# Optimization experiments

Hardware: AMD Instinct MI355X
Metric: run time of the kernel (lower is better)

Reference implementation:

```python
import jax, jax.numpy as jnp
import numpy as np
import math

B, C, H, W, S = 8, 512, 64, 64, 4


def setup_inputs() -> dict:
    key = jax.random.key(0)
    ks = jax.random.split(key, 7)
    s = 1.0 / math.sqrt(C)  # ~ torch Linear init scale
    x = jax.random.normal(ks[0], (B, C, H, W), jnp.float32)
    Wq = jax.random.uniform(ks[1], (C, C), jnp.float32, -s, s)
    bq = jax.random.uniform(ks[2], (C,), jnp.float32, -s, s)
    Wk = jax.random.uniform(ks[3], (C, C), jnp.float32, -s, s)
    bk = jax.random.uniform(ks[4], (C,), jnp.float32, -s, s)
    Wv = jax.random.uniform(ks[5], (C, C), jnp.float32, -s, s)
    bv = jax.random.uniform(ks[6], (C,), jnp.float32, -s, s)
    return {"x": x, "Wq": Wq, "bq": bq, "Wk": Wk, "bk": bk, "Wv": Wv, "bv": bv}


def reference(x, Wq, bq, Wk, bk, Wv, bv):
    # x: (B, C, H, W). Faithful to the torch module's output, but expressed
    # in the algebraically-equivalent efficient form: the repeat_interleaved
    # attention matrix A is block-constant, so out = repeat(A_m @ Vsum).
    b, c, h, w = x.shape
    nb = (h // S) * (w // S)  # number of SxS spatial blocks
    hw = h * w
    ss = S * S

    # Block means in unfold order (bh, bw): (B, nb, C)
    x_avg = x.reshape(b, c, h // S, S, w // S, S).mean(axis=(3, 5))
    x_avg = x_avg.reshape(b, c, nb).transpose(0, 2, 1)

    Q = x_avg @ Wq.T + bq  # (B, nb, C)
    K = x_avg @ Wk.T + bk  # (B, nb, C)
    A = jax.nn.softmax(jnp.einsum('bnc,bmc->bnm', Q, K) / jnp.sqrt(jnp.float32(c)), axis=-1)

    # V over flat row-major pixels: (B, HW, C)
    x_flat = x.reshape(b, c, hw).transpose(0, 2, 1)
    V = x_flat @ Wv.T + bv

    # repeat_interleave on dim=2 means column group j of A sums V rows
    # [j*ss, (j+1)*ss) in FLAT pixel order (not spatial blocks) - faithful.
    Vsum = V.reshape(b, hw // ss, ss, c).sum(axis=2)  # (B, nb, C)
    out_small = jnp.einsum('bnm,bmc->bnc', A, Vsum)   # (B, nb, C)
    # repeat_interleave on dim=1: each block row broadcast to ss flat pixels
    out_flat = jnp.repeat(out_small, ss, axis=1)      # (B, HW, C)
    return out_flat.transpose(0, 2, 1).reshape(b, c, h, w)
```

## Files before the change

kernel.cpp:

```cpp
#include <hip/hip_runtime.h>

typedef __attribute__((ext_vector_type(8))) short short8;
typedef __attribute__((ext_vector_type(4))) float f32x4;

__device__ __forceinline__ unsigned short f2bf(float f) {
    union { float f; unsigned int i; } v; v.f = f;
    unsigned int x = v.i;
    return (unsigned short)((x + 0x7FFFu + ((x >> 16) & 1u)) >> 16);
}
__device__ __forceinline__ f32x4 mfma16(short8 a, short8 b, f32x4 c) {
    return __builtin_amdgcn_mfma_f32_16x16x32_bf16(a, b, c, 0, 0, 0);
}

__global__ void prep_kernel(const float* __restrict__ x,
                            const float* __restrict__ Wq,
                            const float* __restrict__ Wk,
                            const float* __restrict__ Wv,
                            unsigned short* __restrict__ xavg,
                            unsigned short* __restrict__ xsum,
                            unsigned short* __restrict__ Wb)
{
    const int blk = blockIdx.x;
    const int t = threadIdx.x;
    if (blk >= 4096) {
        const int i = (blk - 4096) * 256 + t;
        const int m = i >> 15;
        const int o = (i & 32767) * 8;
        const float* src = (m == 0) ? Wq : (m == 1) ? Wk : Wv;
        unsigned short* dst = Wb + m * 262144 + o;
        float4 a = *(const float4*)(src + o);
        float4 b = *(const float4*)(src + o + 4);
        *(ushort4*)(dst)     = make_ushort4(f2bf(a.x), f2bf(a.y), f2bf(a.z), f2bf(a.w));
        *(ushort4*)(dst + 4) = make_ushort4(f2bf(b.x), f2bf(b.y), f2bf(b.z), f2bf(b.w));
        return;
    }
    const int b = blk >> 9;
    const int c = blk & 511;

    const float4* p = (const float4*)(x + (size_t)blk * 4096) + t * 4;
    float4 a0 = p[0], a1 = p[1], a2 = p[2], a3 = p[3];
    float s0 = a0.x + a0.y + a0.z + a0.w;
    float s1 = a1.x + a1.y + a1.z + a1.w;
    float s2 = a2.x + a2.y + a2.z + a2.w;
    float s3 = a3.x + a3.y + a3.z + a3.w;

    xsum[((size_t)b * 256 + t) * 512 + c] = f2bf(s0 + s1 + s2 + s3);

    __shared__ float part[1024];
    ((float4*)part)[t] = make_float4(s0, s1, s2, s3);
    __syncthreads();

    const int bh = t >> 4, bw = t & 15;
    float m = (part[(bh * 4 + 0) * 16 + bw] + part[(bh * 4 + 1) * 16 + bw] +
               part[(bh * 4 + 2) * 16 + bw] + part[(bh * 4 + 3) * 16 + bw]) * 0.0625f;
    xavg[((size_t)b * 256 + t) * 512 + c] = f2bf(m);
}

__global__ void qk_gemm(const unsigned short* __restrict__ X,
                        const unsigned short* __restrict__ Wqk,
                        const float* __restrict__ bq,
                        const float* __restrict__ bk,
                        unsigned short* __restrict__ QK)
{
    const int wave = blockIdx.x * 4 + (threadIdx.x >> 6);
    const int mt2 = wave >> 5, nt2 = wave & 31;
    const int lane = threadIdx.x & 63, quad = lane >> 4, r16 = lane & 15;
    const unsigned short* xp0 = X + (size_t)(mt2 * 32 + r16) * 512 + quad * 8;
    const unsigned short* xp1 = xp0 + 16 * 512;
    const unsigned short* wp0 = Wqk + (size_t)(nt2 * 32 + r16) * 512 + quad * 8;
    const unsigned short* wp1 = wp0 + 16 * 512;

    f32x4 acc00 = {0,0,0,0}, acc01 = acc00, acc10 = acc00, acc11 = acc00;
#pragma unroll 4
    for (int k = 0; k < 512; k += 32) {
        short8 a0 = *(const short8*)(xp0 + k);
        short8 a1 = *(const short8*)(xp1 + k);
        short8 b0 = *(const short8*)(wp0 + k);
        short8 b1 = *(const short8*)(wp1 + k);
        acc00 = mfma16(a0, b0, acc00);
        acc01 = mfma16(a0, b1, acc01);
        acc10 = mfma16(a1, b0, acc10);
        acc11 = mfma16(a1, b1, acc11);
    }
    const int c0 = nt2 * 32 + r16, c1 = c0 + 16;
    const float bias0 = (c0 < 512) ? bq[c0] : bk[c0 - 512];
    const float bias1 = (c1 < 512) ? bq[c1] : bk[c1 - 512];
    const int row0 = mt2 * 32 + quad * 4;
#pragma unroll
    for (int r = 0; r < 4; ++r) {
        QK[(size_t)(row0 + r) * 1024 + c0]      = f2bf(acc00[r] + bias0);
        QK[(size_t)(row0 + r) * 1024 + c1]      = f2bf(acc01[r] + bias1);
        QK[(size_t)(row0 + 16 + r) * 1024 + c0] = f2bf(acc10[r] + bias0);
        QK[(size_t)(row0 + 16 + r) * 1024 + c1] = f2bf(acc11[r] + bias1);
    }
}

__global__ void v_gemm(const unsigned short* __restrict__ xsum,
                       const unsigned short* __restrict__ Wvb,
                       const float* __restrict__ bv,
                       unsigned short* __restrict__ VsT)
{
    const int b = blockIdx.y;
    const int wave = blockIdx.x * 4 + (threadIdx.x >> 6);
    const int mt2 = wave >> 4, nt2 = wave & 15;
    const int lane = threadIdx.x & 63, quad = lane >> 4, r16 = lane & 15;
    const unsigned short* xp0 = xsum + (size_t)b * 131072 + (size_t)(mt2 * 32 + r16) * 512 + quad * 8;
    const unsigned short* xp1 = xp0 + 16 * 512;
    const unsigned short* wp0 = Wvb + (size_t)(nt2 * 32 + r16) * 512 + quad * 8;
    const unsigned short* wp1 = wp0 + 16 * 512;

    f32x4 acc00 = {0,0,0,0}, acc01 = acc00, acc10 = acc00, acc11 = acc00;
#pragma unroll 4
    for (int k = 0; k < 512; k += 32) {
        short8 a0 = *(const short8*)(xp0 + k);
        short8 a1 = *(const short8*)(xp1 + k);
        short8 b0 = *(const short8*)(wp0 + k);
        short8 b1 = *(const short8*)(wp1 + k);
        acc00 = mfma16(a0, b0, acc00);
        acc01 = mfma16(a0, b1, acc01);
        acc10 = mfma16(a1, b0, acc10);
        acc11 = mfma16(a1, b1, acc11);
    }
    const int c0 = nt2 * 32 + r16, c1 = c0 + 16;
    const float bias0 = 16.f * bv[c0], bias1 = 16.f * bv[c1];
    unsigned short* vb = VsT + (size_t)b * 131072;
    const int m0 = mt2 * 32 + quad * 4;
#pragma unroll
    for (int r = 0; r < 4; ++r) {
        vb[(size_t)c0 * 256 + m0 + r]      = f2bf(acc00[r] + bias0);
        vb[(size_t)c1 * 256 + m0 + r]      = f2bf(acc01[r] + bias1);
        vb[(size_t)c0 * 256 + m0 + 16 + r] = f2bf(acc10[r] + bias0);
        vb[(size_t)c1 * 256 + m0 + 16 + r] = f2bf(acc11[r] + bias1);
    }
}

__global__ void score_softmax(const unsigned short* __restrict__ QK,
                              unsigned short* __restrict__ Amat)
{
    __shared__ float S[32][257];
    const int b = blockIdx.y, strip = blockIdx.x;
    const int w = threadIdx.x >> 6, lane = threadIdx.x & 63;
    const int quad = lane >> 4, r16 = lane & 15;
    const unsigned short* qp0 = QK + (size_t)(b * 256 + strip * 32 + r16) * 1024 + quad * 8;
    const unsigned short* qp1 = qp0 + 16 * 1024;

#pragma unroll
    for (int g = 0; g < 2; ++g) {
        const int ct = w * 2 + g;
        const unsigned short* kp0 = QK + (size_t)(b * 256 + ct * 32 + r16) * 1024 + 512 + quad * 8;
        const unsigned short* kp1 = kp0 + 16 * 1024;
        f32x4 acc00 = {0,0,0,0}, acc01 = acc00, acc10 = acc00, acc11 = acc00;
#pragma unroll 4
        for (int k = 0; k < 512; k += 32) {
            short8 a0 = *(const short8*)(qp0 + k);
            short8 a1 = *(const short8*)(qp1 + k);
            short8 b0 = *(const short8*)(kp0 + k);
            short8 b1 = *(const short8*)(kp1 + k);
            acc00 = mfma16(a0, b0, acc00);
            acc01 = mfma16(a0, b1, acc01);
            acc10 = mfma16(a1, b0, acc10);
            acc11 = mfma16(a1, b1, acc11);
        }
        const int col0 = ct * 32 + r16;
#pragma unroll
        for (int r = 0; r < 4; ++r) {
            S[quad * 4 + r][col0]           = acc00[r];
            S[quad * 4 + r][col0 + 16]      = acc01[r];
            S[quad * 4 + 16 + r][col0]      = acc10[r];
            S[quad * 4 + 16 + r][col0 + 16] = acc11[r];
        }
    }
    __syncthreads();

    const int t = threadIdx.x;
    const int r = t >> 3, seg = t & 7;
    float v[32];
    float mx = -3.4e38f;
#pragma unroll
    for (int j = 0; j < 32; ++j) {
        v[j] = S[r][seg * 32 + j] * 0.044194173824159216f;
        mx = fmaxf(mx, v[j]);
    }
    mx = fmaxf(mx, __shfl_xor(mx, 1));
    mx = fmaxf(mx, __shfl_xor(mx, 2));
    mx = fmaxf(mx, __shfl_xor(mx, 4));
    float sum = 0.f;
#pragma unroll
    for (int j = 0; j < 32; ++j) { v[j] = __expf(v[j] - mx); sum += v[j]; }
    sum += __shfl_xor(sum, 1);
    sum += __shfl_xor(sum, 2);
    sum += __shfl_xor(sum, 4);
    const float inv = 1.f / sum;
    unsigned short* ap = Amat + (size_t)b * 65536 + (size_t)(strip * 32 + r) * 256 + seg * 32;
#pragma unroll
    for (int j = 0; j < 32; j += 4)
        *(ushort4*)(ap + j) = make_ushort4(f2bf(v[j] * inv), f2bf(v[j + 1] * inv),
                                           f2bf(v[j + 2] * inv), f2bf(v[j + 3] * inv));
}

__global__ void av_expand(const unsigned short* __restrict__ Amat,
                          const unsigned short* __restrict__ VsT,
                          float* __restrict__ out)
{
    const int b = blockIdx.y;
    const int wave = blockIdx.x * 4 + (threadIdx.x >> 6);
    const int mt2 = wave >> 4, nt2 = wave & 15;
    const int lane = threadIdx.x & 63, quad = lane >> 4, r16 = lane & 15;
    const unsigned short* ap0 = Amat + (size_t)b * 65536 + (size_t)(mt2 * 32 + r16) * 256 + quad * 8;
    const unsigned short* ap1 = ap0 + 16 * 256;
    const unsigned short* vp0 = VsT + (size_t)b * 131072 + (size_t)(nt2 * 32 + r16) * 256 + quad * 8;
    const unsigned short* vp1 = vp0 + 16 * 256;

    f32x4 acc00 = {0,0,0,0}, acc01 = acc00, acc10 = acc00, acc11 = acc00;
#pragma unroll 4
    for (int k = 0; k < 256; k += 32) {
        short8 a0 = *(const short8*)(ap0 + k);
        short8 a1 = *(const short8*)(ap1 + k);
        short8 b0 = *(const short8*)(vp0 + k);
        short8 b1 = *(const short8*)(vp1 + k);
        acc00 = mfma16(a0, b0, acc00);
        acc01 = mfma16(a0, b1, acc01);
        acc10 = mfma16(a1, b0, acc10);
        acc11 = mfma16(a1, b1, acc11);
    }
    const int c0 = nt2 * 32 + r16, c1 = c0 + 16;
    float* ob0 = out + (size_t)(b * 512 + c0) * 4096;
    float* ob1 = out + (size_t)(b * 512 + c1) * 4096;
    const int n0 = mt2 * 32 + quad * 4;
#pragma unroll
    for (int r = 0; r < 4; ++r) {
        float4 q;
        float4* d;
        q = make_float4(acc00[r], acc00[r], acc00[r], acc00[r]);
        d = (float4*)(ob0 + (n0 + r) * 16);      d[0] = q; d[1] = q; d[2] = q; d[3] = q;
        q = make_float4(acc01[r], acc01[r], acc01[r], acc01[r]);
        d = (float4*)(ob1 + (n0 + r) * 16);      d[0] = q; d[1] = q; d[2] = q; d[3] = q;
        q = make_float4(acc10[r], acc10[r], acc10[r], acc10[r]);
        d = (float4*)(ob0 + (n0 + 16 + r) * 16); d[0] = q; d[1] = q; d[2] = q; d[3] = q;
        q = make_float4(acc11[r], acc11[r], acc11[r], acc11[r]);
        d = (float4*)(ob1 + (n0 + 16 + r) * 16); d[0] = q; d[1] = q; d[2] = q; d[3] = q;
    }
}

extern "C" void kernel_launch(void* const* d_in, const int* in_sizes, int n_in,
                              void* d_out, int out_size, void* d_ws, size_t ws_size,
                              hipStream_t stream) {
    const float* x  = (const float*)d_in[0];
    const float* Wq = (const float*)d_in[1];
    const float* bq = (const float*)d_in[2];
    const float* Wk = (const float*)d_in[3];
    const float* bk = (const float*)d_in[4];
    const float* Wv = (const float*)d_in[5];
    const float* bv = (const float*)d_in[6];
    float* out = (float*)d_out;

    unsigned short* so   = (unsigned short*)d_out;
    unsigned short* Wb   = so;
    unsigned short* xavg = Wb + 786432;
    unsigned short* xsum = xavg + 1048576;
    unsigned short* QK   = xsum + 1048576;
    unsigned short* VsT  = (unsigned short*)d_ws;
    unsigned short* Amat = VsT + 1048576;

    prep_kernel<<<4480, 256, 0, stream>>>(x, Wq, Wk, Wv, xavg, xsum, Wb);
    qk_gemm<<<512, 256, 0, stream>>>(xavg, Wb, bq, bk, QK);
    v_gemm<<<dim3(32, 8), 256, 0, stream>>>(xsum, Wb + 524288, bv, VsT);
    score_softmax<<<dim3(8, 8), 256, 0, stream>>>(QK, Amat);
    av_expand<<<dim3(32, 8), 256, 0, stream>>>(Amat, VsT, out);
}
```

Before: 199.7 us.

## Merge projection GEMMs into one launch and fuse softmax with AV expand

The QK and V projection GEMMs now run as one kernel, with the block index choosing the branch, so they share a single launch. Score computation, softmax and the A·V expand are fused into one kernel, and the attention matrix stays in shared memory instead of going through global memory. To do this, each score strip is recomputed by four blocks, one per quarter of the channels, which repeats the QK^T work four times. All intermediates now live in the workspace rather than partly in the output buffer.

```diff
diff --git a/kernel.cpp b/kernel.cpp
--- a/kernel.cpp
+++ b/kernel.cpp
@@ -56,94 +56,100 @@
     xavg[((size_t)b * 256 + t) * 512 + c] = f2bf(m);
 }
 
-__global__ void qk_gemm(const unsigned short* __restrict__ X,
-                        const unsigned short* __restrict__ Wqk,
-                        const float* __restrict__ bq,
-                        const float* __restrict__ bk,
-                        unsigned short* __restrict__ QK)
+__global__ void proj_gemm(const unsigned short* __restrict__ xavg,
+                          const unsigned short* __restrict__ xsum,
+                          const unsigned short* __restrict__ Wb,
+                          const float* __restrict__ bq,
+                          const float* __restrict__ bk,
+                          const float* __restrict__ bv,
+                          unsigned short* __restrict__ QK,
+                          unsigned short* __restrict__ VsT)
 {
-    const int wave = blockIdx.x * 4 + (threadIdx.x >> 6);
-    const int mt2 = wave >> 5, nt2 = wave & 31;
+    const int blk = blockIdx.x;
     const int lane = threadIdx.x & 63, quad = lane >> 4, r16 = lane & 15;
-    const unsigned short* xp0 = X + (size_t)(mt2 * 32 + r16) * 512 + quad * 8;
-    const unsigned short* xp1 = xp0 + 16 * 512;
-    const unsigned short* wp0 = Wqk + (size_t)(nt2 * 32 + r16) * 512 + quad * 8;
-    const unsigned short* wp1 = wp0 + 16 * 512;
-
-    f32x4 acc00 = {0,0,0,0}, acc01 = acc00, acc10 = acc00, acc11 = acc00;
-#pragma unroll 4
-    for (int k = 0; k < 512; k += 32) {
-        short8 a0 = *(const short8*)(xp0 + k);
-        short8 a1 = *(const short8*)(xp1 + k);
-        short8 b0 = *(const short8*)(wp0 + k);
-        short8 b1 = *(const short8*)(wp1 + k);
-        acc00 = mfma16(a0, b0, acc00);
-        acc01 = mfma16(a0, b1, acc01);
-        acc10 = mfma16(a1, b0, acc10);
-        acc11 = mfma16(a1, b1, acc11);
-    }
-    const int c0 = nt2 * 32 + r16, c1 = c0 + 16;
-    const float bias0 = (c0 < 512) ? bq[c0] : bk[c0 - 512];
-    const float bias1 = (c1 < 512) ? bq[c1] : bk[c1 - 512];
-    const int row0 = mt2 * 32 + quad * 4;
-#pragma unroll
-    for (int r = 0; r < 4; ++r) {
-        QK[(size_t)(row0 + r) * 1024 + c0]      = f2bf(acc00[r] + bias0);
-        QK[(size_t)(row0 + r) * 1024 + c1]      = f2bf(acc01[r] + bias1);
-        QK[(size_t)(row0 + 16 + r) * 1024 + c0] = f2bf(acc10[r] + bias0);
-        QK[(size_t)(row0 + 16 + r) * 1024 + c1] = f2bf(acc11[r] + bias1);
-    }
-}
-
-__global__ void v_gemm(const unsigned short* __restrict__ xsum,
-                       const unsigned short* __restrict__ Wvb,
-                       const float* __restrict__ bv,
-                       unsigned short* __restrict__ VsT)
-{
-    const int b = blockIdx.y;
-    const int wave = blockIdx.x * 4 + (threadIdx.x >> 6);
-    const int mt2 = wave >> 4, nt2 = wave & 15;
-    const int lane = threadIdx.x & 63, quad = lane >> 4, r16 = lane & 15;
-    const unsigned short* xp0 = xsum + (size_t)b * 131072 + (size_t)(mt2 * 32 + r16) * 512 + quad * 8;
-    const unsigned short* xp1 = xp0 + 16 * 512;
-    const unsigned short* wp0 = Wvb + (size_t)(nt2 * 32 + r16) * 512 + quad * 8;
-    const unsigned short* wp1 = wp0 + 16 * 512;
-
-    f32x4 acc00 = {0,0,0,0}, acc01 = acc00, acc10 = acc00, acc11 = acc00;
-#pragma unroll 4
-    for (int k = 0; k < 512; k += 32) {
-        short8 a0 = *(const short8*)(xp0 + k);
-        short8 a1 = *(const short8*)(xp1 + k);
-        short8 b0 = *(const short8*)(wp0 + k);
-        short8 b1 = *(const short8*)(wp1 + k);
-        acc00 = mfma16(a0, b0, acc00);
-        acc01 = mfma16(a0, b1, acc01);
-        acc10 = mfma16(a1, b0, acc10);
-        acc11 = mfma16(a1, b1, acc11);
-    }
-    const int c0 = nt2 * 32 + r16, c1 = c0 + 16;
-    const float bias0 = 16.f * bv[c0], bias1 = 16.f * bv[c1];
-    unsigned short* vb = VsT + (size_t)b * 131072;
-    const int m0 = mt2 * 32 + quad * 4;
-#pragma unroll
-    for (int r = 0; r < 4; ++r) {
-        vb[(size_t)c0 * 256 + m0 + r]      = f2bf(acc00[r] + bias0);
-        vb[(size_t)c1 * 256 + m0 + r]      = f2bf(acc01[r] + bias1);
-        vb[(size_t)c0 * 256 + m0 + 16 + r] = f2bf(acc10[r] + bias0);
-        vb[(size_t)c1 * 256 + m0 + 16 + r] = f2bf(acc11[r] + bias1);
-    }
-}
-
-__global__ void score_softmax(const unsigned short* __restrict__ QK,
-                              unsigned short* __restrict__ Amat)
+    const int w = threadIdx.x >> 6;
+
+    if (blk < 512) {
+        const int wave = blk * 4 + w;
+        const int mt2 = wave >> 5, nt2 = wave & 31;
+        const unsigned short* xp0 = xavg + (size_t)(mt2 * 32 + r16) * 512 + quad * 8;
+        const unsigned short* xp1 = xp0 + 16 * 512;
+        const unsigned short* wp0 = Wb + (size_t)(nt2 * 32 + r16) * 512 + quad * 8;
+        const unsigned short* wp1 = wp0 + 16 * 512;
+
+        f32x4 acc00 = {0,0,0,0}, acc01 = acc00, acc10 = acc00, acc11 = acc00;
+#pragma unroll 4
+        for (int k = 0; k < 512; k += 32) {
+            short8 a0 = *(const short8*)(xp0 + k);
+            short8 a1 = *(const short8*)(xp1 + k);
+            short8 b0 = *(const short8*)(wp0 + k);
+            short8 b1 = *(const short8*)(wp1 + k);
+            acc00 = mfma16(a0, b0, acc00);
+            acc01 = mfma16(a0, b1, acc01);
+            acc10 = mfma16(a1, b0, acc10);
+            acc11 = mfma16(a1, b1, acc11);
+        }
+        const int c0 = nt2 * 32 + r16, c1 = c0 + 16;
+        const float bias0 = (c0 < 512) ? bq[c0] : bk[c0 - 512];
+        const float bias1 = (c1 < 512) ? bq[c1] : bk[c1 - 512];
+        const int row0 = mt2 * 32 + quad * 4;
+#pragma unroll
+        for (int r = 0; r < 4; ++r) {
+            QK[(size_t)(row0 + r) * 1024 + c0]      = f2bf(acc00[r] + bias0);
+            QK[(size_t)(row0 + r) * 1024 + c1]      = f2bf(acc01[r] + bias1);
+            QK[(size_t)(row0 + 16 + r) * 1024 + c0] = f2bf(acc10[r] + bias0);
+            QK[(size_t)(row0 + 16 + r) * 1024 + c1] = f2bf(acc11[r] + bias1);
+        }
+    } else {
+        const int vblk = blk - 512;
+        const int b = vblk >> 5;
+        const int wave = (vblk & 31) * 4 + w;
+        const int mt2 = wave >> 4, nt2 = wave & 15;
+        const unsigned short* xp0 = xsum + (size_t)b * 131072 + (size_t)(mt2 * 32 + r16) * 512 + quad * 8;
+        const unsigned short* xp1 = xp0 + 16 * 512;
+        const unsigned short* wp0 = Wb + 524288 + (size_t)(nt2 * 32 + r16) * 512 + quad * 8;
+        const unsigned short* wp1 = wp0 + 16 * 512;
+
+        f32x4 acc00 = {0,0,0,0}, acc01 = acc00, acc10 = acc00, acc11 = acc00;
+#pragma unroll 4
+        for (int k = 0; k < 512; k += 32) {
+            short8 a0 = *(const short8*)(xp0 + k);
+            short8 a1 = *(const short8*)(xp1 + k);
+            short8 b0 = *(const short8*)(wp0 + k);
+            short8 b1 = *(const short8*)(wp1 + k);
+            acc00 = mfma16(a0, b0, acc00);
+            acc01 = mfma16(a0, b1, acc01);
+            acc10 = mfma16(a1, b0, acc10);
+            acc11 = mfma16(a1, b1, acc11);
+        }
+        const int c0 = nt2 * 32 + r16, c1 = c0 + 16;
+        const float bias0 = 16.f * bv[c0], bias1 = 16.f * bv[c1];
+        unsigned short* vb = VsT + (size_t)b * 131072;
+        const int m0 = mt2 * 32 + quad * 4;
+#pragma unroll
+        for (int r = 0; r < 4; ++r) {
+            vb[(size_t)c0 * 256 + m0 + r]      = f2bf(acc00[r] + bias0);
+            vb[(size_t)c1 * 256 + m0 + r]      = f2bf(acc01[r] + bias1);
+            vb[(size_t)c0 * 256 + m0 + 16 + r] = f2bf(acc10[r] + bias0);
+            vb[(size_t)c1 * 256 + m0 + 16 + r] = f2bf(acc11[r] + bias1);
+        }
+    }
+}
+
+__global__ void attn_out(const unsigned short* __restrict__ QK,
+                         const unsigned short* __restrict__ VsT,
+                         float* __restrict__ out)
 {
     __shared__ float S[32][257];
-    const int b = blockIdx.y, strip = blockIdx.x;
+    __shared__ unsigned short Abf[32 * 264];
+    const int b = blockIdx.y;
+    const int strip = blockIdx.x >> 2;
+    const int cq = blockIdx.x & 3;
     const int w = threadIdx.x >> 6, lane = threadIdx.x & 63;
     const int quad = lane >> 4, r16 = lane & 15;
+
     const unsigned short* qp0 = QK + (size_t)(b * 256 + strip * 32 + r16) * 1024 + quad * 8;
     const unsigned short* qp1 = qp0 + 16 * 1024;
-
 #pragma unroll
     for (int g = 0; g < 2; ++g) {
         const int ct = w * 2 + g;
@@ -172,43 +178,38 @@
     }
     __syncthreads();
 
-    const int t = threadIdx.x;
-    const int r = t >> 3, seg = t & 7;
-    float v[32];
-    float mx = -3.4e38f;
-#pragma unroll
-    for (int j = 0; j < 32; ++j) {
-        v[j] = S[r][seg * 32 + j] * 0.044194173824159216f;
-        mx = fmaxf(mx, v[j]);
-    }
-    mx = fmaxf(mx, __shfl_xor(mx, 1));
-    mx = fmaxf(mx, __shfl_xor(mx, 2));
-    mx = fmaxf(mx, __shfl_xor(mx, 4));
-    float sum = 0.f;
-#pragma unroll
-    for (int j = 0; j < 32; ++j) { v[j] = __expf(v[j] - mx); sum += v[j]; }
-    sum += __shfl_xor(sum, 1);
-    sum += __shfl_xor(sum, 2);
-    sum += __shfl_xor(sum, 4);
-    const float inv = 1.f / sum;
-    unsigned short* ap = Amat + (size_t)b * 65536 + (size_t)(strip * 32 + r) * 256 + seg * 32;
-#pragma unroll
-    for (int j = 0; j < 32; j += 4)
-        *(ushort4*)(ap + j) = make_ushort4(f2bf(v[j] * inv), f2bf(v[j + 1] * inv),
-                                           f2bf(v[j + 2] * inv), f2bf(v[j + 3] * inv));
-}
-
-__global__ void av_expand(const unsigned short* __restrict__ Amat,
-                          const unsigned short* __restrict__ VsT,
-                          float* __restrict__ out)
-{
-    const int b = blockIdx.y;
-    const int wave = blockIdx.x * 4 + (threadIdx.x >> 6);
-    const int mt2 = wave >> 4, nt2 = wave & 15;
-    const int lane = threadIdx.x & 63, quad = lane >> 4, r16 = lane & 15;
-    const unsigned short* ap0 = Amat + (size_t)b * 65536 + (size_t)(mt2 * 32 + r16) * 256 + quad * 8;
-    const unsigned short* ap1 = ap0 + 16 * 256;
-    const unsigned short* vp0 = VsT + (size_t)b * 131072 + (size_t)(nt2 * 32 + r16) * 256 + quad * 8;
+    {
+        const int t = threadIdx.x;
+        const int r = t >> 3, seg = t & 7;
+        float v[32];
+        float mx = -3.4e38f;
+#pragma unroll
+        for (int j = 0; j < 32; ++j) {
+            v[j] = S[r][seg * 32 + j] * 0.044194173824159216f;
+            mx = fmaxf(mx, v[j]);
+        }
+        mx = fmaxf(mx, __shfl_xor(mx, 1));
+        mx = fmaxf(mx, __shfl_xor(mx, 2));
+        mx = fmaxf(mx, __shfl_xor(mx, 4));
+        float sum = 0.f;
+#pragma unroll
+        for (int j = 0; j < 32; ++j) { v[j] = __expf(v[j] - mx); sum += v[j]; }
+        sum += __shfl_xor(sum, 1);
+        sum += __shfl_xor(sum, 2);
+        sum += __shfl_xor(sum, 4);
+        const float inv = 1.f / sum;
+        unsigned short* ap = Abf + r * 264 + seg * 32;
+#pragma unroll
+        for (int j = 0; j < 32; j += 4)
+            *(ushort4*)(ap + j) = make_ushort4(f2bf(v[j] * inv), f2bf(v[j + 1] * inv),
+                                               f2bf(v[j + 2] * inv), f2bf(v[j + 3] * inv));
+    }
+    __syncthreads();
+
+    const int cbase = cq * 128 + w * 32;
+    const unsigned short* ap0 = Abf + r16 * 264 + quad * 8;
+    const unsigned short* ap1 = ap0 + 16 * 264;
+    const unsigned short* vp0 = VsT + (size_t)b * 131072 + (size_t)(cbase + r16) * 256 + quad * 8;
     const unsigned short* vp1 = vp0 + 16 * 256;
 
     f32x4 acc00 = {0,0,0,0}, acc01 = acc00, acc10 = acc00, acc11 = acc00;
@@ -223,10 +224,10 @@
         acc10 = mfma16(a1, b0, acc10);
         acc11 = mfma16(a1, b1, acc11);
     }
-    const int c0 = nt2 * 32 + r16, c1 = c0 + 16;
+    const int c0 = cbase + r16, c1 = c0 + 16;
     float* ob0 = out + (size_t)(b * 512 + c0) * 4096;
     float* ob1 = out + (size_t)(b * 512 + c1) * 4096;
-    const int n0 = mt2 * 32 + quad * 4;
+    const int n0 = strip * 32 + quad * 4;
 #pragma unroll
     for (int r = 0; r < 4; ++r) {
         float4 q;
@@ -254,17 +255,13 @@
     const float* bv = (const float*)d_in[6];
     float* out = (float*)d_out;
 
-    unsigned short* so   = (unsigned short*)d_out;
-    unsigned short* Wb   = so;
+    unsigned short* Wb   = (unsigned short*)d_ws;
     unsigned short* xavg = Wb + 786432;
     unsigned short* xsum = xavg + 1048576;
     unsigned short* QK   = xsum + 1048576;
-    unsigned short* VsT  = (unsigned short*)d_ws;
-    unsigned short* Amat = VsT + 1048576;
+    unsigned short* VsT  = QK + 2097152;
 
     prep_kernel<<<4480, 256, 0, stream>>>(x, Wq, Wk, Wv, xavg, xsum, Wb);
-    qk_gemm<<<512, 256, 0, stream>>>(xavg, Wb, bq, bk, QK);
-    v_gemm<<<dim3(32, 8), 256, 0, stream>>>(xsum, Wb + 524288, bv, VsT);
-    score_softmax<<<dim3(8, 8), 256, 0, stream>>>(QK, Amat);
-    av_expand<<<dim3(32, 8), 256, 0, stream>>>(Amat, VsT, out);
-}
+    proj_gemm<<<768, 256, 0, stream>>>(xavg, xsum, Wb, bq, bk, bv, QK, VsT);
+    attn_out<<<dim3(32, 8), 256, 0, stream>>>(QK, VsT, out);
+}
```

Result: faster. 193.2 us (-3.2%).
